# Kernel tuning notes

Measured on AMD Instinct MI355X. Metric: run time of the kernel, lower is better.

The kernel has to match this reference:

```python
import jax, jax.numpy as jnp
import numpy as np

N, E, D = 50000, 800000, 128
BN_EPS = 1e-5


def mish(x):
    return x * jnp.tanh(jax.nn.softplus(x))


def setup_inputs() -> dict:
    key = jax.random.key(0)
    ks = jax.random.split(key, 16)
    s = 1.0 / np.sqrt(D)
    s2 = 1.0 / np.sqrt(2 * D)
    # unique (row, col) edge pairs so the dense-adjacency edge norm reduces
    # exactly to conv_w[bond_type] + conv_b per edge
    rng = np.random.default_rng(0)
    codes = np.unique(rng.integers(0, N * N, size=2 * E, dtype=np.int64))[:E]
    edge_index = jnp.asarray(np.stack([codes // N, codes % N]), dtype=jnp.int32)
    bond_types = jnp.asarray(rng.integers(0, 4, size=E), dtype=jnp.int32)

    def nrm(k, shape, sc):
        return jax.random.normal(k, shape, jnp.float32) * sc

    return {
        "x": nrm(ks[0], (N, D), 1.0),
        "coords": nrm(ks[1], (N, 3), 1.0),
        "edge_index": edge_index,
        "bond_types": bond_types,
        # NodeFeaturePath
        "W_nb": nrm(ks[2], (2 * D, D), s2), "b_nb": jnp.zeros((D,), jnp.float32),
        "W_nout": nrm(ks[3], (D, D), s), "b_nout": jnp.zeros((D,), jnp.float32),
        # EdgeFeaturePath (1x1 conv over 4 bond-type channels -> scalar per edge)
        "conv_w": nrm(ks[4], (4,), 0.5), "conv_b": jnp.zeros((), jnp.float32),
        "W_el": nrm(ks[5], (2 * D, D), s2), "b_el": jnp.zeros((D,), jnp.float32),
        "W_eout": nrm(ks[6], (D, D), s), "b_eout": jnp.zeros((D,), jnp.float32),
        # StructuralFeaturePath
        "W_coord": nrm(ks[7], (2 * D, D), s2), "b_coord": jnp.zeros((D,), jnp.float32),
        "W_pair": nrm(ks[8], (D, D), s), "b_pair": jnp.zeros((D,), jnp.float32),
        "W_sout": nrm(ks[9], (2 * D, D), s2), "b_sout": jnp.zeros((D,), jnp.float32),
        # FeatureAggregation (att mode, all bias-free)
        "W_init": nrm(ks[10], (D, D), s),
        "feat_lin": nrm(ks[11], (3, D, D), s),
        "W_att": nrm(ks[12], (2 * D, D), s2),
        "W_agg": nrm(ks[13], (D, D), s),
        # BatchNorm (training mode)
        "gamma": jnp.ones((D,), jnp.float32), "beta": jnp.zeros((D,), jnp.float32),
    }


def _forward(x, coords, edge_index, bond_types,
             W_nb, b_nb, W_nout, b_nout,
             conv_w, conv_b, W_el, b_el, W_eout, b_eout,
             W_coord, b_coord, W_pair, b_pair, W_sout, b_sout,
             W_init, feat_lin, W_att, W_agg, gamma, beta):
    act = mish
    src, dst = edge_index[0], edge_index[1]  # PyG: x_j = x[src], x_i = x[dst]
    pair = jnp.concatenate([x[dst], x[src]], axis=1)  # [E, 2D] = [x_i, x_j]

    # --- node path ---
    msg = act(pair @ W_nb + b_nb)                                  # [E, D]
    P = jax.ops.segment_sum(msg, dst, num_segments=N)              # [N, D]
    f_node = act(P @ W_nout + b_nout)

    # --- edge path: 1x1 conv over one-hot bond-type adjacency == lookup ---
    norm_e = (conv_w[bond_types] + conv_b)[:, None]                # [E, 1]
    msg = act((norm_e * pair) @ W_el + b_el)
    P = jax.ops.segment_sum(msg, dst, num_segments=N)
    f_edge = act(P @ W_eout + b_eout)

    # --- struct path ---
    d2 = jnp.sum((coords[src] - coords[dst]) ** 2, axis=1, keepdims=True)  # [E,1]
    msg = (d2 * pair) @ W_coord + b_coord                          # no act in message
    Q = jax.ops.segment_sum(msg, dst, num_segments=N)
    Q = act(Q @ W_pair + b_pair)
    f_struct = act(jnp.concatenate([x, Q], axis=1) @ W_sout + b_sout)

    # --- attention aggregation over the 3 feature paths ---
    feat_stack = jnp.stack([f_node, f_edge, f_struct], axis=0)     # [3, N, D]
    lin_init = act(x @ W_init)[None]                               # [1, N, D] (broadcast of repeat)
    lin_feats = act(jnp.einsum('fnd,fde->fne', feat_stack, feat_lin))
    h = act(jnp.concatenate([jnp.broadcast_to(lin_init, lin_feats.shape), lin_feats], axis=2))
    e = h @ W_att                                                  # [3, N, D]
    a = jax.nn.softmax(e, axis=0)
    att = jnp.sum(a * feat_stack, axis=0)                          # einsum fnd,fnd->nd
    h_agg = att @ W_agg

    # --- batchnorm (training stats, biased var) + final activation ---
    mean = h_agg.mean(axis=0)
    var = h_agg.var(axis=0)
    h_bn = (h_agg - mean) / jnp.sqrt(var + BN_EPS) * gamma + beta
    return act(h_bn)  # final=False


def reference(x, coords, edge_index, bond_types,
              W_nb, b_nb, W_nout, b_nout,
              conv_w, conv_b, W_el, b_el, W_eout, b_eout,
              W_coord, b_coord, W_pair, b_pair, W_sout, b_sout,
              W_init, feat_lin, W_att, W_agg, gamma, beta):
    return _forward(x, coords, edge_index, bond_types,
                    W_nb, b_nb, W_nout, b_nout,
                    conv_w, conv_b, W_el, b_el, W_eout, b_eout,
                    W_coord, b_coord, W_pair, b_pair, W_sout, b_sout,
                    W_init, feat_lin, W_att, W_agg, gamma, beta)
```

## Files before the change

### kernel.cpp

```cpp
#include <hip/hip_runtime.h>
#include <math.h>

#define DD 128
#define LDSS 136
#define PLANE (16 * LDSS)
#define WT 16384

typedef __attribute__((ext_vector_type(8))) short bf16x8;
typedef __attribute__((ext_vector_type(4))) float f32x4;
typedef unsigned short u16;
typedef unsigned int u32;
struct u32x3 { u32 x, y, z; };

__device__ __forceinline__ u16 f2bf(float f) {
    u32 u = __builtin_bit_cast(u32, f);
    u += 0x7fffu + ((u >> 16) & 1u);
    return (u16)(u >> 16);
}
__device__ __forceinline__ float bf2f(u16 h) {
    u32 u = ((u32)h) << 16;
    return __builtin_bit_cast(float, u);
}
__device__ __forceinline__ float mishf(float x) {
    float e = __expf(fminf(x, 15.0f));
    float n = e * (e + 2.0f);
    return x * n * __builtin_amdgcn_rcpf(n + 2.0f);
}
__device__ __forceinline__ void splitv(float v, u16& h, u16& l) {
    u32 u = __builtin_bit_cast(u32, v);
    h = (u16)(u >> 16);
    float r = v - __builtin_bit_cast(float, u & 0xffff0000u);
    l = (u16)(__builtin_bit_cast(u32, r) >> 16);
}

__device__ __forceinline__ void zero2(f32x4* acc) {
    f32x4 z4 = {0.f, 0.f, 0.f, 0.f};
    acc[0] = z4; acc[1] = z4;
}

__device__ __forceinline__ void prefetchB4(const u16* __restrict__ Wh, const u16* __restrict__ Wl,
                                           int lane, int ntB, bf16x8* pre)
{
    size_t b0 = (((size_t)ntB + 0) * 64 + lane) * 8;
    size_t b1 = (((size_t)ntB + 1) * 64 + lane) * 8;
    pre[0] = *(const bf16x8*)(Wh + b0);
    pre[1] = *(const bf16x8*)(Wl + b0);
    pre[2] = *(const bf16x8*)(Wh + b1);
    pre[3] = *(const bf16x8*)(Wl + b1);
}

template<int NM, bool SPLIT = false>
__device__ __forceinline__ void gemm2(const bf16x8* ah, const bf16x8* al,
    const u16* __restrict__ Wh, const u16* __restrict__ Wl, int lane, int ntB, f32x4* acc)
{
    f32x4 accB[2];
    if (SPLIT) zero2(accB);
#pragma unroll
    for (int kb = 0; kb < 4; kb++)
#pragma unroll
        for (int j = 0; j < 2; j++) {
            size_t boff = (((size_t)kb * 8 + ntB + j) * 64 + lane) * 8;
            f32x4* ac = (SPLIT && (kb & 1)) ? accB : acc;
            bf16x8 bh = *(const bf16x8*)(Wh + boff);
            ac[j] = __builtin_amdgcn_mfma_f32_16x16x32_bf16(ah[kb], bh, ac[j], 0, 0, 0);
            if (NM >= 2) {
                bf16x8 bl = *(const bf16x8*)(Wl + boff);
                ac[j] = __builtin_amdgcn_mfma_f32_16x16x32_bf16(ah[kb], bl, ac[j], 0, 0, 0);
            }
            if (NM == 3)
                ac[j] = __builtin_amdgcn_mfma_f32_16x16x32_bf16(al[kb], bh, ac[j], 0, 0, 0);
        }
    if (SPLIT) {
        acc[0] += accB[0];
        acc[1] += accB[1];
    }
}

template<int NM, bool SPLIT = false>
__device__ __forceinline__ void gemm2_pre(const bf16x8* ah, const bf16x8* al,
    const u16* __restrict__ Wh, const u16* __restrict__ Wl, int lane, int ntB,
    f32x4* acc, const bf16x8* pre)
{
    f32x4 accB[2];
    if (SPLIT) zero2(accB);
#pragma unroll
    for (int kb = 0; kb < 4; kb++)
#pragma unroll
        for (int j = 0; j < 2; j++) {
            size_t boff = (((size_t)kb * 8 + ntB + j) * 64 + lane) * 8;
            f32x4* ac = (SPLIT && (kb & 1)) ? accB : acc;
            bf16x8 bh = (kb == 0) ? pre[j * 2] : *(const bf16x8*)(Wh + boff);
            ac[j] = __builtin_amdgcn_mfma_f32_16x16x32_bf16(ah[kb], bh, ac[j], 0, 0, 0);
            if (NM >= 2) {
                bf16x8 bl = (kb == 0) ? pre[j * 2 + 1] : *(const bf16x8*)(Wl + boff);
                ac[j] = __builtin_amdgcn_mfma_f32_16x16x32_bf16(ah[kb], bl, ac[j], 0, 0, 0);
            }
            if (NM == 3)
                ac[j] = __builtin_amdgcn_mfma_f32_16x16x32_bf16(al[kb], bh, ac[j], 0, 0, 0);
        }
    if (SPLIT) {
        acc[0] += accB[0];
        acc[1] += accB[1];
    }
}

__device__ __forceinline__ void gemm2_dual_pre(const bf16x8* a1, const bf16x8* a2,
    const u16* __restrict__ W1h, const u16* __restrict__ W1l,
    const u16* __restrict__ W2h, const u16* __restrict__ W2l,
    int lane, int ntB, f32x4* acc1, f32x4* acc2, const bf16x8* pre)
{
#pragma unroll
    for (int kb = 0; kb < 4; kb++)
#pragma unroll
        for (int j = 0; j < 2; j++) {
            size_t boff = (((size_t)kb * 8 + ntB + j) * 64 + lane) * 8;
            bf16x8 b1h = (kb == 0) ? pre[j * 2]     : *(const bf16x8*)(W1h + boff);
            bf16x8 b1l = (kb == 0) ? pre[j * 2 + 1] : *(const bf16x8*)(W1l + boff);
            acc1[j] = __builtin_amdgcn_mfma_f32_16x16x32_bf16(a1[kb], b1h, acc1[j], 0, 0, 0);
            acc1[j] = __builtin_amdgcn_mfma_f32_16x16x32_bf16(a1[kb], b1l, acc1[j], 0, 0, 0);
            bf16x8 b2h = (W2h == W1h) ? b1h : *(const bf16x8*)(W2h + boff);
            bf16x8 b2l = (W2l == W1l) ? b1l : *(const bf16x8*)(W2l + boff);
            acc2[j] = __builtin_amdgcn_mfma_f32_16x16x32_bf16(a2[kb], b2h, acc2[j], 0, 0, 0);
            acc2[j] = __builtin_amdgcn_mfma_f32_16x16x32_bf16(a2[kb], b2l, acc2[j], 0, 0, 0);
        }
}

__device__ __forceinline__ void frag_hi_global16(const u16* __restrict__ src, int row0,
                                                 int lm, int quad, int M, bf16x8* ah)
{
    int row = row0 + lm; if (row >= M) row = M - 1;
    const u16* p = src + (size_t)row * DD + quad * 8;
#pragma unroll
    for (int kb = 0; kb < 4; kb++) ah[kb] = *(const bf16x8*)(p + kb * 32);
}
__device__ __forceinline__ void frag_split_global16(const float* __restrict__ src, int row0,
                                                    int lm, int quad, int M, bf16x8* ah, bf16x8* al)
{
    int row = row0 + lm; if (row >= M) row = M - 1;
    const float* p = src + (size_t)row * DD + quad * 8;
#pragma unroll
    for (int kb = 0; kb < 4; kb++) {
        float tmp[8];
        *(float4*)tmp       = *(const float4*)(p + kb * 32);
        *(float4*)(tmp + 4) = *(const float4*)(p + kb * 32 + 4);
#pragma unroll
        for (int j = 0; j < 8; j++) { u16 h, l; splitv(tmp[j], h, l); ah[kb][j] = (short)h; al[kb][j] = (short)l; }
    }
}
__device__ __forceinline__ void frag_hi_plane16(const u16* P, int lm, int quad, bf16x8* ah)
{
    const u16* p = P + (size_t)lm * LDSS + quad * 8;
#pragma unroll
    for (int kb = 0; kb < 4; kb++) ah[kb] = *(const bf16x8*)(p + kb * 32);
}
__device__ __forceinline__ void frag_planes16(const u16* PH, const u16* PL, int lm, int quad,
                                              bf16x8* ah, bf16x8* al)
{
    const u16* ph = PH + (size_t)lm * LDSS + quad * 8;
    const u16* pl = PL + (size_t)lm * LDSS + quad * 8;
#pragma unroll
    for (int kb = 0; kb < 4; kb++) {
        ah[kb] = *(const bf16x8*)(ph + kb * 32);
        al[kb] = *(const bf16x8*)(pl + kb * 32);
    }
}

struct WSrc { const float* p[18]; };

__global__ __launch_bounds__(256) void prep_weights(WSrc ws, u16* __restrict__ Wh, u16* __restrict__ Wl)
{
    int mat = blockIdx.x >> 3, chunk = blockIdx.x & 7;
    int t = threadIdx.x;
    int tt = chunk * 4 + (t >> 6);
    int lane = t & 63;
    int kb = tt >> 3, nt = tt & 7;
    const float* __restrict__ src = ws.p[mat];
    size_t doff = (size_t)mat * WT + ((size_t)tt * 64 + lane) * 8;
    int srow = kb * 32 + ((lane >> 4) * 8);
    int scol = nt * 16 + (lane & 15);
    u16 th[8], tl[8];
#pragma unroll
    for (int j = 0; j < 8; j++) {
        float v = src[(srow + j) * DD + scol];
        u16 h = f2bf(v);
        th[j] = h;
        tl[j] = f2bf(v - bf2f(h));
    }
    *(bf16x8*)(Wh + doff) = *(bf16x8*)th;
    *(bf16x8*)(Wl + doff) = *(bf16x8*)tl;
}

__global__ __launch_bounds__(256, 4) void fronthist_kernel(
    const float* __restrict__ x, const u16* __restrict__ Wh, const u16* __restrict__ Wl,
    u16* __restrict__ G, u16* __restrict__ xWs,
    float* __restrict__ At, float* __restrict__ Bt, float* __restrict__ Ct,
    const int* __restrict__ ei, int* __restrict__ deg, int E, int M, int NBF)
{
    __shared__ u16 sP[3 * PLANE];
    const int t = threadIdx.x;
    if ((int)blockIdx.x >= NBF) {
        int e = ((int)blockIdx.x - NBF) * 256 + t;
        if (e < E) atomicAdd(&deg[ei[E + e]], 1);
        return;
    }
    u16 *P0 = sP, *P1 = sP + PLANE, *P2 = sP + 2 * PLANE;
    const int wave = t >> 6, lane = t & 63;
    const int lm = lane & 15, quad = lane >> 4;
    const int ntB = wave * 2;
    const int row0 = blockIdx.x * 16;

    bf16x8 ah[4], al[4];
    {
        int row = row0 + lm; if (row >= M) row = M - 1;
        const float* p = x + (size_t)row * DD + quad * 8;
#pragma unroll
        for (int kb = 0; kb < 4; kb++) {
            float tmp[8];
            *(float4*)tmp       = *(const float4*)(p + kb * 32);
            *(float4*)(tmp + 4) = *(const float4*)(p + kb * 32 + 4);
#pragma unroll
            for (int j = 0; j < 8; j++) {
                u16 h, l; splitv(tmp[j], h, l);
                ah[kb][j] = (short)h; al[kb][j] = (short)l;
                if (wave == 0) P0[lm * LDSS + kb * 32 + quad * 8 + j] = f2bf(tmp[j]);
            }
        }
    }
    {
        f32x4 acc[2]; zero2(acc);
        gemm2<1>(ah, ah, Wh + 1 * WT, Wh, lane, ntB, acc);
#pragma unroll
        for (int r = 0; r < 4; r++)
#pragma unroll
            for (int j = 0; j < 2; j++)
                P1[(quad * 4 + r) * LDSS + (ntB + j) * 16 + lm] = f2bf(acc[j][r]);
    }
    {
        f32x4 acc[2]; zero2(acc);
        gemm2<1>(ah, ah, Wh + 3 * WT, Wh, lane, ntB, acc);
#pragma unroll
        for (int r = 0; r < 4; r++)
#pragma unroll
            for (int j = 0; j < 2; j++)
                P2[(quad * 4 + r) * LDSS + (ntB + j) * 16 + lm] = f2bf(acc[j][r]);
    }
    __syncthreads();
#pragma unroll
    for (int i = 0; i < 4; i++) {
        int r = wave * 4 + i;
        int grow = row0 + r;
        if (grow >= M) continue;
        u16* gp = G + (size_t)grow * 384 + lane * 6;
        u32x3 v;
        v.x = *(const u32*)&P1[r * LDSS + lane * 2];
        v.y = *(const u32*)&P2[r * LDSS + lane * 2];
        v.z = *(const u32*)&P0[r * LDSS + lane * 2];
        *(u32x3*)gp = v;
    }
    {
        f32x4 acc[2]; zero2(acc);
        gemm2<1>(ah, ah, Wh + 5 * WT, Wh, lane, ntB, acc);
#pragma unroll
        for (int r = 0; r < 4; r++) {
            int grow = row0 + quad * 4 + r;
            if (grow >= M) continue;
#pragma unroll
            for (int j = 0; j < 2; j++)
                xWs[(size_t)grow * DD + (ntB + j) * 16 + lm] = f2bf(acc[j][r]);
        }
    }
    {
        float* outs[3] = {At, Bt, Ct};
        const int mats[3] = {0, 2, 4};
#pragma unroll
        for (int wi = 0; wi < 3; wi++) {
            f32x4 acc[2]; zero2(acc);
            gemm2<3>(ah, al, Wh + (size_t)mats[wi] * WT, Wl + (size_t)mats[wi] * WT, lane, ntB, acc);
            float* out = outs[wi];
#pragma unroll
            for (int r = 0; r < 4; r++) {
                int grow = row0 + quad * 4 + r;
                if (grow >= M) continue;
#pragma unroll
                for (int j = 0; j < 2; j++)
                    out[(size_t)grow * DD + (ntB + j) * 16 + lm] = acc[j][r];
            }
        }
    }
}

__global__ __launch_bounds__(1024) void scan_kernel(const int* __restrict__ deg,
                                                    int* __restrict__ rowptr,
                                                    int* __restrict__ cursor, int N)
{
    __shared__ int sums[1024];
    const int CH = 52;
    int t = threadIdx.x;
    int base = t * CH;
    int local = 0;
#pragma unroll
    for (int i = 0; i < 13; i++) {
        int idx = base + i * 4;
        if (idx + 3 < N) {
            int4 v = *(const int4*)(deg + idx);
            local += v.x + v.y + v.z + v.w;
        } else {
            for (int k = 0; k < 4; k++) if (idx + k < N) local += deg[idx + k];
        }
    }
    sums[t] = local;
    __syncthreads();
    for (int off = 1; off < 1024; off <<= 1) {
        int v = sums[t];
        int u = (t >= off) ? sums[t - off] : 0;
        __syncthreads();
        sums[t] = v + u;
        __syncthreads();
    }
    int run = (t == 0) ? 0 : sums[t - 1];
    for (int i = 0; i < CH; i++) {
        int idx = base + i;
        if (idx < N) {
            rowptr[idx] = run;
            cursor[idx] = run;
            run += deg[idx];
        }
    }
    if (t == 1023) rowptr[N] = sums[1023];
}

__global__ __launch_bounds__(256) void scatter_kernel(
    const int* __restrict__ ei, const int* __restrict__ bond,
    const float* __restrict__ coords, int* __restrict__ cursor,
    int2* __restrict__ csr, int E)
{
    int e = blockIdx.x * 256 + threadIdx.x;
    if (e >= E) return;
    int src = ei[e], dst = ei[E + e];
    int pos = atomicAdd(&cursor[dst], 1);
    float dx = coords[src * 3 + 0] - coords[dst * 3 + 0];
    float dy = coords[src * 3 + 1] - coords[dst * 3 + 1];
    float dz = coords[src * 3 + 2] - coords[dst * 3 + 2];
    float d2 = dx * dx + dy * dy + dz * dz;
    csr[pos] = make_int2(src | (bond[e] << 20), __float_as_int(d2));
}

__global__ __launch_bounds__(256) void edge_agg(
    const float* __restrict__ At, const float* __restrict__ Bt,
    const u16* __restrict__ G,
    const int* __restrict__ rowptr, const int2* __restrict__ csr,
    const float* __restrict__ conv_w, const float* __restrict__ conv_b,
    const float* __restrict__ b_nb, const float* __restrict__ b_el,
    u16* __restrict__ Pn, u16* __restrict__ Pe, float* __restrict__ z,
    float* __restrict__ s_arr, int N)
{
    int wave = threadIdx.x >> 6;
    int lane = threadIdx.x & 63;
    int node = blockIdx.x * 4 + wave;
    if (node >= N) return;
    int c0 = lane * 2;
    int lane6 = lane * 6;
    float2 at = *(const float2*)(At + (size_t)node * DD + c0);
    float2 bt = *(const float2*)(Bt + (size_t)node * DD + c0);
    float cb = conv_b[0];
    float cw0 = conv_w[0] + cb, cw1 = conv_w[1] + cb, cw2 = conv_w[2] + cb, cw3 = conv_w[3] + cb;
    float bn0 = b_nb[c0], bn1 = b_nb[c0 + 1];
    float be0 = b_el[c0], be1 = b_el[c0 + 1];
    float accn0 = 0.f, accn1 = 0.f, acce0 = 0.f, acce1 = 0.f, accz0 = 0.f, accz1 = 0.f, ssum = 0.f;
    int beg = rowptr[node], end = rowptr[node + 1];

    auto consume = [&](int px, float d2, u32 ga, u32 gb, u32 gx) {
        int bondv = (px >> 20) & 3;
        float w = (bondv == 0) ? cw0 : (bondv == 1) ? cw1 : (bondv == 2) ? cw2 : cw3;
        float a0 = __builtin_bit_cast(float, ga << 16), a1 = __builtin_bit_cast(float, ga & 0xffff0000u);
        float b0 = __builtin_bit_cast(float, gb << 16), b1 = __builtin_bit_cast(float, gb & 0xffff0000u);
        float x0 = __builtin_bit_cast(float, gx << 16), x1 = __builtin_bit_cast(float, gx & 0xffff0000u);
        accn0 += mishf(at.x + a0 + bn0);
        accn1 += mishf(at.y + a1 + bn1);
        acce0 += mishf(w * (bt.x + b0) + be0);
        acce1 += mishf(w * (bt.y + b1) + be1);
        accz0 += d2 * x0;
        accz1 += d2 * x1;
        ssum += d2;
    };

    int k = beg;
    for (; k + 8 <= end; k += 8) {
        int2 pd[8];
        u32x3 g[8];
#pragma unroll
        for (int i = 0; i < 8; i++) pd[i] = csr[k + i];
#pragma unroll
        for (int i = 0; i < 8; i++)
            g[i] = *(const u32x3*)(G + (size_t)(pd[i].x & 0xFFFFF) * 384 + lane6);
#pragma unroll
        for (int i = 0; i < 8; i++)
            consume(pd[i].x, __int_as_float(pd[i].y), g[i].x, g[i].y, g[i].z);
    }
    for (; k + 4 <= end; k += 4) {
        int2 pd[4];
        u32x3 g[4];
#pragma unroll
        for (int i = 0; i < 4; i++) pd[i] = csr[k + i];
#pragma unroll
        for (int i = 0; i < 4; i++)
            g[i] = *(const u32x3*)(G + (size_t)(pd[i].x & 0xFFFFF) * 384 + lane6);
#pragma unroll
        for (int i = 0; i < 4; i++)
            consume(pd[i].x, __int_as_float(pd[i].y), g[i].x, g[i].y, g[i].z);
    }
    for (; k < end; k++) {
        int2 pd = csr[k];
        u32x3 g = *(const u32x3*)(G + (size_t)(pd.x & 0xFFFFF) * 384 + lane6);
        consume(pd.x, __int_as_float(pd.y), g.x, g.y, g.z);
    }

    *(u32*)(Pn + (size_t)node * DD + c0) = (u32)f2bf(accn0) | ((u32)f2bf(accn1) << 16);
    *(u32*)(Pe + (size_t)node * DD + c0) = (u32)f2bf(acce0) | ((u32)f2bf(acce1) << 16);
    *(float2*)(z + (size_t)node * DD + c0) = make_float2(accz0, accz1);
    if (lane == 0) s_arr[node] = ssum;
}

__global__ __launch_bounds__(256, 3) void mega_kernel(
    const u16* __restrict__ Pn, const u16* __restrict__ Pe, const float* __restrict__ z,
    const float* __restrict__ Ct, const u16* __restrict__ xWs,
    const float* __restrict__ s_arr, const int* __restrict__ deg,
    const float* __restrict__ b_nout, const float* __restrict__ b_eout,
    const float* __restrict__ b_coord, const float* __restrict__ b_pair,
    const float* __restrict__ b_sout,
    const u16* __restrict__ Wh, const u16* __restrict__ Wl,
    float* __restrict__ hout, float* __restrict__ bnsums, int M)
{
    __shared__ u16 sP[4 * PLANE];
    u16 *PA = sP, *PB = sP + PLANE, *PC = sP + 2 * PLANE, *PD = sP + 3 * PLANE;
    const int t = threadIdx.x, wave = t >> 6, lane = t & 63;
    const int lm = lane & 15, quad = lane >> 4;
    const int ntB = wave * 2;
    const int row0 = blockIdx.x * 16;

    u32 f1p[4], f2p[4], f3p[4];
    float d1v[8], d2v[8];
    bf16x8 preB[4];

    {
        bf16x8 an[4], ae[4];
        f32x4 accn[2], acce[2];
        prefetchB4(Wh + 11 * WT, Wl + 11 * WT, lane, ntB, preB);
        frag_hi_global16(Pn, row0, lm, quad, M, an);
        frag_hi_global16(Pe, row0, lm, quad, M, ae);
        zero2(accn); zero2(acce);
        gemm2_dual_pre(an, ae, Wh + 11 * WT, Wl + 11 * WT, Wh + 12 * WT, Wl + 12 * WT, lane, ntB, accn, acce, preB);
#pragma unroll
        for (int r = 0; r < 4; r++) {
            u32 pkn = 0, pke = 0;
#pragma unroll
            for (int j = 0; j < 2; j++) {
                int col = (ntB + j) * 16 + lm;
                int lidx = (quad * 4 + r) * LDSS + col;
                u16 hn = f2bf(mishf(accn[j][r] + b_nout[col]));
                u16 he = f2bf(mishf(acce[j][r] + b_eout[col]));
                pkn |= ((u32)hn) << (16 * j);
                pke |= ((u32)he) << (16 * j);
                PA[lidx] = hn; PB[lidx] = he;
            }
            f1p[r] = pkn; f2p[r] = pke;
        }
        prefetchB4(Wh + 13 * WT, Wl + 13 * WT, lane, ntB, preB);
        __syncthreads();
        frag_hi_plane16(PA, lm, quad, an);
        frag_hi_plane16(PB, lm, quad, ae);
        zero2(accn); zero2(acce);
        gemm2_dual_pre(an, ae, Wh + 13 * WT, Wl + 13 * WT, Wh + 14 * WT, Wl + 14 * WT, lane, ntB, accn, acce, preB);
#pragma unroll
        for (int r = 0; r < 4; r++)
#pragma unroll
            for (int j = 0; j < 2; j++) {
                int lidx = (quad * 4 + r) * LDSS + (ntB + j) * 16 + lm;
                PC[lidx] = f2bf(mishf(mishf(accn[j][r])));
                PD[lidx] = f2bf(mishf(mishf(acce[j][r])));
            }
        prefetchB4(Wh + 16 * WT, Wl + 16 * WT, lane, ntB, preB);
        __syncthreads();
        frag_hi_plane16(PC, lm, quad, an);
        frag_hi_plane16(PD, lm, quad, ae);
        zero2(accn); zero2(acce);
        gemm2_dual_pre(an, ae, Wh + 16 * WT, Wl + 16 * WT, Wh + 16 * WT, Wl + 16 * WT, lane, ntB, accn, acce, preB);
#pragma unroll
        for (int r = 0; r < 4; r++)
#pragma unroll
            for (int j = 0; j < 2; j++) {
                d1v[r * 2 + j] = accn[j][r];
                d2v[r * 2 + j] = acce[j][r];
            }
    }

    bf16x8 ah[4], al[4];
    f32x4 acc[2];
    prefetchB4(Wh + 8 * WT, Wl + 8 * WT, lane, ntB, preB);
    frag_split_global16(z, row0, lm, quad, M, ah, al);
    zero2(acc);
    gemm2_pre<3, true>(ah, al, Wh + 8 * WT, Wl + 8 * WT, lane, ntB, acc, preB);
#pragma unroll
    for (int r = 0; r < 4; r++) {
        int crow = row0 + quad * 4 + r; if (crow >= M) crow = M - 1;
        float sv = s_arr[crow];
        float dv = (float)deg[crow];
#pragma unroll
        for (int j = 0; j < 2; j++) {
            int col = (ntB + j) * 16 + lm;
            float v = acc[j][r] + sv * Ct[(size_t)crow * DD + col] + dv * b_coord[col];
            int lidx = (quad * 4 + r) * LDSS + col;
            u16 h, l; splitv(v, h, l); PA[lidx] = h; PB[lidx] = l;
        }
    }
    prefetchB4(Wh + 9 * WT, Wl + 9 * WT, lane, ntB, preB);
    __syncthreads();
    frag_planes16(PA, PB, lm, quad, ah, al);
    zero2(acc);
    gemm2_pre<3, true>(ah, al, Wh + 9 * WT, Wl + 9 * WT, lane, ntB, acc, preB);
#pragma unroll
    for (int r = 0; r < 4; r++)
#pragma unroll
        for (int j = 0; j < 2; j++) {
            int col = (ntB + j) * 16 + lm;
            int lidx = (quad * 4 + r) * LDSS + col;
            u16 h, l; splitv(mishf(acc[j][r] + b_pair[col]), h, l); PC[lidx] = h; PD[lidx] = l;
        }
    prefetchB4(Wh + 10 * WT, Wl + 10 * WT, lane, ntB, preB);
    __syncthreads();
    frag_planes16(PC, PD, lm, quad, ah, al);
    zero2(acc);
    gemm2_pre<3, true>(ah, al, Wh + 10 * WT, Wl + 10 * WT, lane, ntB, acc, preB);
#pragma unroll
    for (int r = 0; r < 4; r++) {
        int crow = row0 + quad * 4 + r; if (crow >= M) crow = M - 1;
        u32 pk = 0;
#pragma unroll
        for (int j = 0; j < 2; j++) {
            int col = (ntB + j) * 16 + lm;
            float v = mishf(acc[j][r] + bf2f(xWs[(size_t)crow * DD + col]) + b_sout[col]);
            u16 h, l; splitv(v, h, l);
            pk |= ((u32)f2bf(v)) << (16 * j);
            int lidx = (quad * 4 + r) * LDSS + col;
            PA[lidx] = h; PB[lidx] = l;
        }
        f3p[r] = pk;
    }
    prefetchB4(Wh + 15 * WT, Wl + 15 * WT, lane, ntB, preB);
    __syncthreads();
    frag_planes16(PA, PB, lm, quad, ah, al);
    zero2(acc);
    gemm2_pre<3, true>(ah, al, Wh + 15 * WT, Wl + 15 * WT, lane, ntB, acc, preB);
#pragma unroll
    for (int r = 0; r < 4; r++)
#pragma unroll
        for (int j = 0; j < 2; j++) {
            int lidx = (quad * 4 + r) * LDSS + (ntB + j) * 16 + lm;
            u16 h, l; splitv(mishf(mishf(acc[j][r])), h, l); PC[lidx] = h; PD[lidx] = l;
        }
    prefetchB4(Wh + 16 * WT, Wl + 16 * WT, lane, ntB, preB);
    __syncthreads();
    frag_planes16(PC, PD, lm, quad, ah, al);
    zero2(acc);
    gemm2_pre<3, true>(ah, al, Wh + 16 * WT, Wl + 16 * WT, lane, ntB, acc, preB);

#pragma unroll
    for (int r = 0; r < 4; r++)
#pragma unroll
        for (int j = 0; j < 2; j++) {
            int i = r * 2 + j;
            float x1 = d1v[i], x2 = d2v[i], x3 = acc[j][r];
            float m = fmaxf(fmaxf(x1, x2), x3);
            float p1 = __expf(x1 - m), p2 = __expf(x2 - m), p3 = __expf(x3 - m);
            float fv1 = bf2f((u16)(f1p[r] >> (16 * j)));
            float fv2 = bf2f((u16)(f2p[r] >> (16 * j)));
            float fv3 = bf2f((u16)(f3p[r] >> (16 * j)));
            float att = (p1 * fv1 + p2 * fv2 + p3 * fv3) * __builtin_amdgcn_rcpf(p1 + p2 + p3);
            int lidx = (quad * 4 + r) * LDSS + (ntB + j) * 16 + lm;
            u16 h, l; splitv(att, h, l); PA[lidx] = h; PB[lidx] = l;
        }
    prefetchB4(Wh + 17 * WT, Wl + 17 * WT, lane, ntB, preB);
    __syncthreads();
    frag_planes16(PA, PB, lm, quad, ah, al);
    zero2(acc);
    gemm2_pre<3, true>(ah, al, Wh + 17 * WT, Wl + 17 * WT, lane, ntB, acc, preB);
    float s[2] = {0.f, 0.f}, q[2] = {0.f, 0.f};
#pragma unroll
    for (int r = 0; r < 4; r++) {
        int grow = row0 + quad * 4 + r;
        if (grow >= M) continue;
#pragma unroll
        for (int j = 0; j < 2; j++) {
            float v = acc[j][r];
            hout[(size_t)grow * DD + (ntB + j) * 16 + lm] = v;
            s[j] += v; q[j] += v * v;
        }
    }
    __syncthreads();
    float* red = (float*)sP;
    if (t < 128) { red[t] = 0.f; red[128 + t] = 0.f; }
    __syncthreads();
#pragma unroll
    for (int j = 0; j < 2; j++) {
        int col = (ntB + j) * 16 + lm;
        atomicAdd(&red[col], s[j]);
        atomicAdd(&red[128 + col], q[j]);
    }
    __syncthreads();
    if (t < 128) {
        atomicAdd(&bnsums[t], red[t]);
        atomicAdd(&bnsums[128 + t], red[128 + t]);
    }
}

__global__ void bn_finalize(const float* __restrict__ sums, const float* __restrict__ gamma,
                            const float* __restrict__ beta, float* __restrict__ scale,
                            float* __restrict__ shift, float n_inv)
{
    int c = threadIdx.x;
    float mean = sums[c] * n_inv;
    float var = sums[128 + c] * n_inv - mean * mean;
    float inv = rsqrtf(var + 1e-5f);
    float sc = gamma[c] * inv;
    scale[c] = sc;
    shift[c] = beta[c] - mean * sc;
}

__global__ __launch_bounds__(256) void bn_apply(float* __restrict__ h, const float* __restrict__ scale,
                                                const float* __restrict__ shift, size_t total4)
{
    size_t idx = (size_t)blockIdx.x * 256 + threadIdx.x;
    if (idx >= total4) return;
    size_t off = idx * 4;
    int c = (int)(off & 127);
    float4 v = *(const float4*)(h + off);
    float4 sc = *(const float4*)(scale + c);
    float4 sh = *(const float4*)(shift + c);
    v.x = mishf(v.x * sc.x + sh.x);
    v.y = mishf(v.y * sc.y + sh.y);
    v.z = mishf(v.z * sc.z + sh.z);
    v.w = mishf(v.w * sc.w + sh.w);
    *(float4*)(h + off) = v;
}

extern "C" void kernel_launch(void* const* d_in, const int* in_sizes, int n_in,
                              void* d_out, int out_size, void* d_ws, size_t ws_size,
                              hipStream_t stream)
{
    (void)n_in; (void)out_size; (void)ws_size;
    const float* x       = (const float*)d_in[0];
    const float* coords  = (const float*)d_in[1];
    const int*   ei      = (const int*)d_in[2];
    const int*   bond    = (const int*)d_in[3];
    const float* W_nb    = (const float*)d_in[4];
    const float* b_nb    = (const float*)d_in[5];
    const float* W_nout  = (const float*)d_in[6];
    const float* b_nout  = (const float*)d_in[7];
    const float* conv_w  = (const float*)d_in[8];
    const float* conv_b  = (const float*)d_in[9];
    const float* W_el    = (const float*)d_in[10];
    const float* b_el    = (const float*)d_in[11];
    const float* W_eout  = (const float*)d_in[12];
    const float* b_eout  = (const float*)d_in[13];
    const float* W_coord = (const float*)d_in[14];
    const float* b_coord = (const float*)d_in[15];
    const float* W_pair  = (const float*)d_in[16];
    const float* b_pair  = (const float*)d_in[17];
    const float* W_sout  = (const float*)d_in[18];
    const float* b_sout  = (const float*)d_in[19];
    const float* W_init  = (const float*)d_in[20];
    const float* feat_lin= (const float*)d_in[21];
    const float* W_att   = (const float*)d_in[22];
    const float* W_agg   = (const float*)d_in[23];
    const float* gamma   = (const float*)d_in[24];
    const float* beta    = (const float*)d_in[25];

    const int N = in_sizes[0] / DD;
    const int E = in_sizes[3];
    const size_t ND = (size_t)N * DD;
    const int SUB = DD * DD;
    const int NB16 = (N + 15) / 16;
    const int EB   = (E + 255) / 256;

    char* base = (char*)d_ws;
    size_t off = 0;
    auto alloc = [&](size_t bytes) -> char* {
        char* p = base + off;
        off = (off + bytes + 63) & ~(size_t)63;
        return p;
    };
    u16*   G    = (u16*)alloc((size_t)N * 384 * 2);
    u16*   xWs  = (u16*)alloc(ND * 2);
    float* At   = (float*)alloc(ND * 4);
    float* Bt   = (float*)alloc(ND * 4);
    float* Ct   = (float*)alloc(ND * 4);
    u16*   Pn   = (u16*)alloc(ND * 2);
    u16*   Pe   = (u16*)alloc(ND * 2);
    float* z    = (float*)alloc(ND * 4);
    u16*   Wh   = (u16*)alloc((size_t)18 * WT * 2);
    u16*   Wl   = (u16*)alloc((size_t)18 * WT * 2);
    int2*  csr  = (int2*)alloc((size_t)E * 8);
    int*   deg    = (int*)alloc((size_t)(N + 64) * 4);
    int*   rowptr = (int*)alloc((size_t)(N + 1) * 4);
    int*   cursor = (int*)alloc((size_t)N * 4);
    float* s_arr  = (float*)alloc((size_t)N * 4);
    float* bnsums  = (float*)alloc(256 * 4);
    float* bnscale = (float*)alloc(128 * 4);
    float* bnshift = (float*)alloc(128 * 4);

    float* hout = (float*)d_out;

    WSrc wsrc;
    wsrc.p[0] = W_nb;            wsrc.p[1] = W_nb + SUB;
    wsrc.p[2] = W_el;            wsrc.p[3] = W_el + SUB;
    wsrc.p[4] = W_coord;         wsrc.p[5] = W_sout;
    wsrc.p[6] = W_init;          wsrc.p[7] = W_att;
    wsrc.p[8] = W_coord + SUB;   wsrc.p[9] = W_pair;
    wsrc.p[10] = W_sout + SUB;   wsrc.p[11] = W_nout;
    wsrc.p[12] = W_eout;         wsrc.p[13] = feat_lin;
    wsrc.p[14] = feat_lin + SUB; wsrc.p[15] = feat_lin + 2 * SUB;
    wsrc.p[16] = W_att + SUB;    wsrc.p[17] = W_agg;

    const dim3 blk256(256);
    const size_t total4 = ND / 4;
    const dim3 gElem((unsigned)((total4 + 255) / 256));

    hipMemsetAsync(deg, 0, (size_t)N * 4, stream);
    hipMemsetAsync(bnsums, 0, 256 * 4, stream);

    prep_weights<<<dim3(18 * 8), blk256, 0, stream>>>(wsrc, Wh, Wl);
    fronthist_kernel<<<dim3(NB16 + EB), blk256, 0, stream>>>(x, Wh, Wl, G, xWs, At, Bt, Ct,
                                                             ei, deg, E, N, NB16);
    scan_kernel<<<1, 1024, 0, stream>>>(deg, rowptr, cursor, N);
    scatter_kernel<<<dim3(EB), blk256, 0, stream>>>(ei, bond, coords, cursor, csr, E);

    edge_agg<<<(N + 3) / 4, blk256, 0, stream>>>(At, Bt, G, rowptr, csr, conv_w, conv_b,
                                                 b_nb, b_el, Pn, Pe, z, s_arr, N);

    mega_kernel<<<NB16, blk256, 0, stream>>>(Pn, Pe, z, Ct, xWs, s_arr, deg,
                                             b_nout, b_eout, b_coord, b_pair, b_sout,
                                             Wh, Wl, hout, bnsums, N);

    bn_finalize<<<1, 128, 0, stream>>>(bnsums, gamma, beta, bnscale, bnshift, 1.0f / (float)N);
    bn_apply<<<gElem, blk256, 0, stream>>>(hout, bnscale, bnshift, total4);
}
```

Baseline: 603.1 us.

## Replace single-block degree scan with three-phase multi-block scan

The exclusive prefix sum over node degrees, which ran in a single 1024-thread block, is split into three kernels: per-tile partial sums, a one-wavefront scan of tile totals, and a per-tile fill that writes rowptr and cursor. This spreads the scan across many compute units instead of serialising it on one. The cost is two extra kernel launches. The tile-offset scan handles at most 64 tiles (65536 nodes), which covers N=50000.

```diff
diff --git a/kernel.cpp b/kernel.cpp
--- a/kernel.cpp
+++ b/kernel.cpp
@@ -5,6 +5,7 @@
 #define LDSS 136
 #define PLANE (16 * LDSS)
 #define WT 16384
+#define SCAN_TILE 1024
 
 typedef __attribute__((ext_vector_type(8))) short bf16x8;
 typedef __attribute__((ext_vector_type(4))) float f32x4;
@@ -289,44 +290,77 @@
     }
 }
 
-__global__ __launch_bounds__(1024) void scan_kernel(const int* __restrict__ deg,
-                                                    int* __restrict__ rowptr,
-                                                    int* __restrict__ cursor, int N)
-{
-    __shared__ int sums[1024];
-    const int CH = 52;
+__global__ __launch_bounds__(256) void scan_partial(const int* __restrict__ deg,
+                                                    int* __restrict__ bsum, int N)
+{
     int t = threadIdx.x;
-    int base = t * CH;
-    int local = 0;
-#pragma unroll
-    for (int i = 0; i < 13; i++) {
-        int idx = base + i * 4;
-        if (idx + 3 < N) {
-            int4 v = *(const int4*)(deg + idx);
-            local += v.x + v.y + v.z + v.w;
-        } else {
-            for (int k = 0; k < 4; k++) if (idx + k < N) local += deg[idx + k];
-        }
-    }
-    sums[t] = local;
-    __syncthreads();
-    for (int off = 1; off < 1024; off <<= 1) {
-        int v = sums[t];
-        int u = (t >= off) ? sums[t - off] : 0;
+    int base = blockIdx.x * SCAN_TILE + t * 4;
+    int s = 0;
+    if (base + 3 < N) {
+        int4 v = *(const int4*)(deg + base);
+        s = v.x + v.y + v.z + v.w;
+    } else {
+        for (int i = 0; i < 4; i++) if (base + i < N) s += deg[base + i];
+    }
+    __shared__ int red[256];
+    red[t] = s;
+    __syncthreads();
+    for (int off = 128; off > 0; off >>= 1) {
+        if (t < off) red[t] += red[t + off];
         __syncthreads();
-        sums[t] = v + u;
+    }
+    if (t == 0) bsum[blockIdx.x] = red[0];
+}
+
+__global__ __launch_bounds__(64) void scan_mid(const int* __restrict__ bsum,
+                                               int* __restrict__ boff,
+                                               int* __restrict__ rowptr, int nblk, int N)
+{
+    int l = threadIdx.x;
+    int mine = (l < nblk) ? bsum[l] : 0;
+    int v = mine;
+    for (int off = 1; off < 64; off <<= 1) {
+        int u = __shfl_up(v, off);
+        if (l >= off) v += u;
+    }
+    if (l < nblk) boff[l] = v - mine;
+    if (l == 63) rowptr[N] = v;
+}
+
+__global__ __launch_bounds__(256) void scan_fill(const int* __restrict__ deg,
+                                                 const int* __restrict__ boff,
+                                                 int* __restrict__ rowptr,
+                                                 int* __restrict__ cursor, int N)
+{
+    int t = threadIdx.x;
+    int base = blockIdx.x * SCAN_TILE + t * 4;
+    int d[4] = {0, 0, 0, 0};
+    if (base + 3 < N) {
+        int4 v = *(const int4*)(deg + base);
+        d[0] = v.x; d[1] = v.y; d[2] = v.z; d[3] = v.w;
+    } else {
+        for (int i = 0; i < 4; i++) if (base + i < N) d[i] = deg[base + i];
+    }
+    int s = d[0] + d[1] + d[2] + d[3];
+    __shared__ int pf[256];
+    pf[t] = s;
+    __syncthreads();
+    for (int off = 1; off < 256; off <<= 1) {
+        int v = pf[t];
+        int u = (t >= off) ? pf[t - off] : 0;
         __syncthreads();
-    }
-    int run = (t == 0) ? 0 : sums[t - 1];
-    for (int i = 0; i < CH; i++) {
+        pf[t] = v + u;
+        __syncthreads();
+    }
+    int run = boff[blockIdx.x] + pf[t] - s;
+    for (int i = 0; i < 4; i++) {
         int idx = base + i;
         if (idx < N) {
             rowptr[idx] = run;
             cursor[idx] = run;
-            run += deg[idx];
-        }
-    }
-    if (t == 1023) rowptr[N] = sums[1023];
+            run += d[i];
+        }
+    }
 }
 
 __global__ __launch_bounds__(256) void scatter_kernel(
@@ -681,6 +715,7 @@
     const int SUB = DD * DD;
     const int NB16 = (N + 15) / 16;
     const int EB   = (E + 255) / 256;
+    const int NSCAN = (N + SCAN_TILE - 1) / SCAN_TILE;
 
     char* base = (char*)d_ws;
     size_t off = 0;
@@ -704,6 +739,8 @@
     int*   rowptr = (int*)alloc((size_t)(N + 1) * 4);
     int*   cursor = (int*)alloc((size_t)N * 4);
     float* s_arr  = (float*)alloc((size_t)N * 4);
+    int*   bsum   = (int*)alloc((size_t)(NSCAN + 64) * 4);
+    int*   boff   = (int*)alloc((size_t)(NSCAN + 64) * 4);
     float* bnsums  = (float*)alloc(256 * 4);
     float* bnscale = (float*)alloc(128 * 4);
     float* bnshift = (float*)alloc(128 * 4);
@@ -731,7 +768,9 @@
     prep_weights<<<dim3(18 * 8), blk256, 0, stream>>>(wsrc, Wh, Wl);
     fronthist_kernel<<<dim3(NB16 + EB), blk256, 0, stream>>>(x, Wh, Wl, G, xWs, At, Bt, Ct,
                                                              ei, deg, E, N, NB16);
-    scan_kernel<<<1, 1024, 0, stream>>>(deg, rowptr, cursor, N);
+    scan_partial<<<dim3(NSCAN), blk256, 0, stream>>>(deg, bsum, N);
+    scan_mid<<<1, 64, 0, stream>>>(bsum, boff, rowptr, NSCAN, N);
+    scan_fill<<<dim3(NSCAN), blk256, 0, stream>>>(deg, boff, rowptr, cursor, N);
     scatter_kernel<<<dim3(EB), blk256, 0, stream>>>(ei, bond, coords, cursor, csr, E);
 
     edge_agg<<<(N + 3) / 4, blk256, 0, stream>>>(At, Bt, G, rowptr, csr, conv_w, conv_b,
```

Measured after the change: 509.2 us. 1.18x faster.
